# Optimization experiments

Measured on AMD Instinct MI355X. Metric: run time of the kernel, lower is better.

Reference implementation:

```python
import jax, jax.numpy as jnp
import numpy as np

N_NODES = 50000
N_EDGES = 640000
D_IN = 128
D_OUT = 128


def setup_inputs() -> dict:
    key = jax.random.key(0)
    k1, k2, k3, k4 = jax.random.split(key, 4)
    x = jax.random.normal(k1, (N_NODES, D_IN), dtype=jnp.float32)
    edge_index = jax.random.randint(k2, (2, N_EDGES), 0, N_NODES, dtype=jnp.int64)
    weight = jax.random.uniform(k3, (1,), dtype=jnp.float32)
    temperature = jnp.ones((1,), dtype=jnp.float32)
    W = jax.random.normal(k4, (D_IN, D_OUT), dtype=jnp.float32) * (1.0 / np.sqrt(D_IN))
    b = jnp.zeros((D_OUT,), dtype=jnp.float32)
    return {"x": x, "edge_index": edge_index, "weight": weight,
            "temperature": temperature, "W": W, "b": b}


def _gcn_conv(x, edge_index, W, b):
    N = x.shape[0]
    src, dst = edge_index[0], edge_index[1]
    loop = jnp.arange(N, dtype=edge_index.dtype)
    s = jnp.concatenate([src, loop])  # self-loops appended
    d = jnp.concatenate([dst, loop])
    deg = jax.ops.segment_sum(jnp.ones(s.shape[0], dtype=x.dtype), d, num_segments=N)
    dinv = jnp.where(deg > 0, deg ** -0.5, 0.0)
    norm = dinv[s] * dinv[d]  # [E+N]
    h = x @ W                 # linear transform first (PyG GCNConv)
    msg = h[s] * norm[:, None]
    out = jax.ops.segment_sum(msg, d, num_segments=N)
    return out + b


def _gradient_entropy(x, edge_index, temperature):
    # Boltzmann distribution over per-node Dirichlet energies;
    # entropy gradient w.r.t. node features (computed with autodiff).
    N = x.shape[0]
    src, dst = edge_index[0], edge_index[1]

    def entropy(z):
        diff = z[src] - z[dst]                                  # [E, D]
        E = jax.ops.segment_sum(jnp.sum(diff * diff, axis=-1), dst, num_segments=N)
        logp = jax.nn.log_softmax(-E / temperature[0])
        p = jnp.exp(logp)
        return -jnp.sum(p * logp)

    return jax.grad(entropy)(x)


def reference(x, edge_index, weight, temperature, W, b):
    h = _gcn_conv(x, edge_index, W, b)
    g = jax.lax.stop_gradient(_gradient_entropy(h, edge_index, temperature))
    return h + weight * g
```

## Files before the change

kernel.cpp:

```cpp
#include <hip/hip_runtime.h>

#define N_NODES 50000
#define N_EDGES 640000
#define NSCANB  196
#define MAXD    64

#define OFF_HTMPB    0
#define OFF_OBF      3200000
#define OFF_CURSOR   6400000
#define OFF_E        6450000
#define OFF_PMIN     6500000
#define OFF_PS0      6500256
#define OFF_PS1      6500512
#define OFF_WT       6500768
#define OFF_EBIN     6508960

typedef __attribute__((ext_vector_type(8))) short bf16x8;
typedef __attribute__((ext_vector_type(4))) float f32x4;

__device__ __forceinline__ unsigned short f2bf(float f) {
    unsigned u = __float_as_uint(f);
    unsigned r = u + 0x7fffu + ((u >> 16) & 1u);
    return (unsigned short)(r >> 16);
}
__device__ __forceinline__ float bflo(unsigned u) { return __uint_as_float(u << 16); }
__device__ __forceinline__ float bfhi(unsigned u) { return __uint_as_float(u & 0xffff0000u); }

__global__ __launch_bounds__(256) void k_init(const float* __restrict__ W,
                                              int* __restrict__ cursor,
                                              unsigned short* __restrict__ wtg) {
    int gtid = blockIdx.x * 256 + threadIdx.x;
    if (gtid < N_NODES) cursor[gtid] = 0;
    if (gtid < 4096) {
        int k = gtid >> 5, n4 = (gtid & 31) * 4;
        float4 v = *(const float4*)(W + k * 128 + n4);
        wtg[(n4 + 0) * 128 + k] = f2bf(v.x);
        wtg[(n4 + 1) * 128 + k] = f2bf(v.y);
        wtg[(n4 + 2) * 128 + k] = f2bf(v.z);
        wtg[(n4 + 3) * 128 + k] = f2bf(v.w);
    }
}

__global__ __launch_bounds__(256) void k_gemm(const float* __restrict__ x,
                                              const unsigned short* __restrict__ wtg,
                                              unsigned short* __restrict__ htmpb) {
    int tid = threadIdx.x;
    int wave = tid >> 6, lane = tid & 63, quad = lane >> 4, m16 = lane & 15;
    int r0 = blockIdx.x * 32 + (wave & 1) * 16;
    int ch = (wave >> 1) * 4;
    int arow = r0 + m16;
    int rowc = arow < N_NODES ? arow : N_NODES - 1;
    f32x4 acc[4];
    #pragma unroll
    for (int c = 0; c < 4; c++) acc[c] = (f32x4){0.f, 0.f, 0.f, 0.f};
    #pragma unroll
    for (int kt = 0; kt < 4; kt++) {
        int koff = kt * 32 + quad * 8;
        float4 xa = *(const float4*)(x + rowc * 128 + koff);
        float4 xb = *(const float4*)(x + rowc * 128 + koff + 4);
        bf16x8 af;
        af[0] = (short)f2bf(xa.x); af[1] = (short)f2bf(xa.y);
        af[2] = (short)f2bf(xa.z); af[3] = (short)f2bf(xa.w);
        af[4] = (short)f2bf(xb.x); af[5] = (short)f2bf(xb.y);
        af[6] = (short)f2bf(xb.z); af[7] = (short)f2bf(xb.w);
        #pragma unroll
        for (int c = 0; c < 4; c++) {
            bf16x8 bfrag = *(const bf16x8*)(wtg + ((ch + c) * 16 + m16) * 128 + koff);
            acc[c] = __builtin_amdgcn_mfma_f32_16x16x32_bf16(af, bfrag, acc[c], 0, 0, 0);
        }
    }
    #pragma unroll
    for (int reg = 0; reg < 4; reg++) {
        int grow = r0 + quad * 4 + reg;
        if (grow < N_NODES) {
            #pragma unroll
            for (int c = 0; c < 4; c++)
                htmpb[grow * 128 + (ch + c) * 16 + m16] = f2bf(acc[c][reg]);
        }
    }
}

__global__ __launch_bounds__(256) void k_bucket(const int* __restrict__ src,
                                                const int* __restrict__ dst,
                                                int* __restrict__ cursor,
                                                int* __restrict__ ebin) {
    int e = blockIdx.x * 256 + threadIdx.x;
    int d = dst[e];
    int pos = atomicAdd(&cursor[d], 1);
    if (pos < MAXD) ebin[d * MAXD + pos] = src[e];
}

__global__ __launch_bounds__(256) void k_gather(const unsigned short* __restrict__ htmpb,
                                                const int* __restrict__ deg,
                                                const float* __restrict__ b,
                                                const int* __restrict__ ebin,
                                                float* __restrict__ out,
                                                unsigned short* __restrict__ obf) {
    int node = blockIdx.x * 8 + (threadIdx.x >> 5);
    int lane = threadIdx.x & 31;
    int dg = deg[node]; if (dg > MAXD) dg = MAXD;
    float di = rsqrtf((float)(dg + 1));
    float4 bv = *(const float4*)(b + lane * 4);
    uint2 hv = *(const uint2*)(htmpb + node * 128 + lane * 4);
    float sl = di * di;
    float ax = bv.x + bflo(hv.x) * sl, ay = bv.y + bfhi(hv.x) * sl;
    float az = bv.z + bflo(hv.y) * sl, aw = bv.w + bfhi(hv.y) * sl;
    float cx = 0.f, cy = 0.f, cz = 0.f, cw = 0.f;
    const int* bin = ebin + node * MAXD;
    int k = 0;
    for (; k + 3 < dg; k += 4) {
        int s0 = bin[k], s1 = bin[k + 1], s2 = bin[k + 2], s3 = bin[k + 3];
        float n0 = di * rsqrtf((float)(deg[s0] + 1));
        float n1 = di * rsqrtf((float)(deg[s1] + 1));
        float n2 = di * rsqrtf((float)(deg[s2] + 1));
        float n3 = di * rsqrtf((float)(deg[s3] + 1));
        uint2 u0 = *(const uint2*)(htmpb + s0 * 128 + lane * 4);
        uint2 u1 = *(const uint2*)(htmpb + s1 * 128 + lane * 4);
        uint2 u2 = *(const uint2*)(htmpb + s2 * 128 + lane * 4);
        uint2 u3 = *(const uint2*)(htmpb + s3 * 128 + lane * 4);
        ax += bflo(u0.x) * n0; ay += bfhi(u0.x) * n0;
        az += bflo(u0.y) * n0; aw += bfhi(u0.y) * n0;
        cx += bflo(u1.x) * n1; cy += bfhi(u1.x) * n1;
        cz += bflo(u1.y) * n1; cw += bfhi(u1.y) * n1;
        ax += bflo(u2.x) * n2; ay += bfhi(u2.x) * n2;
        az += bflo(u2.y) * n2; aw += bfhi(u2.y) * n2;
        cx += bflo(u3.x) * n3; cy += bfhi(u3.x) * n3;
        cz += bflo(u3.y) * n3; cw += bfhi(u3.y) * n3;
    }
    for (; k < dg; k++) {
        int s0 = bin[k];
        float n0 = di * rsqrtf((float)(deg[s0] + 1));
        uint2 u0 = *(const uint2*)(htmpb + s0 * 128 + lane * 4);
        ax += bflo(u0.x) * n0; ay += bfhi(u0.x) * n0;
        az += bflo(u0.y) * n0; aw += bfhi(u0.y) * n0;
    }
    ax += cx; ay += cy; az += cz; aw += cw;
    *(float4*)(out + node * 128 + lane * 4) = make_float4(ax, ay, az, aw);
    uint2 pk;
    pk.x = (unsigned)f2bf(ax) | ((unsigned)f2bf(ay) << 16);
    pk.y = (unsigned)f2bf(az) | ((unsigned)f2bf(aw) << 16);
    *(uint2*)(obf + node * 128 + lane * 4) = pk;
}

__global__ __launch_bounds__(256) void k_energy(const unsigned short* __restrict__ obf,
                                                const int* __restrict__ deg,
                                                const int* __restrict__ ebin,
                                                float* __restrict__ E) {
    int node = blockIdx.x * 8 + (threadIdx.x >> 5);
    int lane = threadIdx.x & 31;
    int dg = deg[node]; if (dg > MAXD) dg = MAXD;
    uint2 ud = *(const uint2*)(obf + node * 128 + lane * 4);
    float o0 = bflo(ud.x), o1 = bfhi(ud.x), o2 = bflo(ud.y), o3 = bfhi(ud.y);
    float acc = 0.f, acc2 = 0.f;
    const int* bin = ebin + node * MAXD;
    int k = 0;
    for (; k + 3 < dg; k += 4) {
        int s0 = bin[k], s1 = bin[k + 1], s2 = bin[k + 2], s3 = bin[k + 3];
        uint2 a = *(const uint2*)(obf + s0 * 128 + lane * 4);
        uint2 c = *(const uint2*)(obf + s1 * 128 + lane * 4);
        uint2 g = *(const uint2*)(obf + s2 * 128 + lane * 4);
        uint2 h = *(const uint2*)(obf + s3 * 128 + lane * 4);
        float d0 = bflo(a.x) - o0, d1 = bfhi(a.x) - o1, d2 = bflo(a.y) - o2, d3 = bfhi(a.y) - o3;
        float e4 = bflo(c.x) - o0, e5 = bfhi(c.x) - o1, e6 = bflo(c.y) - o2, e7 = bfhi(c.y) - o3;
        float f0 = bflo(g.x) - o0, f1 = bfhi(g.x) - o1, f2 = bflo(g.y) - o2, f3 = bfhi(g.y) - o3;
        float h4 = bflo(h.x) - o0, h5 = bfhi(h.x) - o1, h6 = bflo(h.y) - o2, h7 = bfhi(h.y) - o3;
        acc  += d0 * d0 + d1 * d1 + d2 * d2 + d3 * d3;
        acc2 += e4 * e4 + e5 * e5 + e6 * e6 + e7 * e7;
        acc  += f0 * f0 + f1 * f1 + f2 * f2 + f3 * f3;
        acc2 += h4 * h4 + h5 * h5 + h6 * h6 + h7 * h7;
    }
    for (; k < dg; k++) {
        int s0 = bin[k];
        uint2 a = *(const uint2*)(obf + s0 * 128 + lane * 4);
        float d0 = bflo(a.x) - o0, d1 = bfhi(a.x) - o1, d2 = bflo(a.y) - o2, d3 = bfhi(a.y) - o3;
        acc += d0 * d0 + d1 * d1 + d2 * d2 + d3 * d3;
    }
    acc += acc2;
    #pragma unroll
    for (int off = 16; off; off >>= 1) acc += __shfl_xor(acc, off);
    if (lane == 0) E[node] = acc;
}

__global__ __launch_bounds__(256) void k_esoft(const float* __restrict__ E,
                                               const float* __restrict__ temp,
                                               float* __restrict__ pmin,
                                               float* __restrict__ ps0,
                                               float* __restrict__ ps1) {
    __shared__ float fred[12];
    int tid = threadIdx.x;
    int i = blockIdx.x * 256 + tid;
    int lane = tid & 63, wid = tid >> 6;
    float e = (i < N_NODES) ? E[i] : 3.402823466e38f;
    float m = e;
    #pragma unroll
    for (int off = 32; off; off >>= 1) m = fminf(m, __shfl_xor(m, off));
    if (lane == 0) fred[wid] = m;
    __syncthreads();
    float bm = fminf(fminf(fred[0], fred[1]), fminf(fred[2], fred[3]));
    float T = temp[0];
    float s0 = 0.f, s1 = 0.f;
    if (i < N_NODES) {
        float dd = (bm - e) / T;
        float ed = __expf(dd);
        s0 = ed; s1 = ed * dd;
    }
    #pragma unroll
    for (int off = 32; off; off >>= 1) { s0 += __shfl_xor(s0, off); s1 += __shfl_xor(s1, off); }
    __syncthreads();
    if (lane == 0) { fred[4 + wid] = s0; fred[8 + wid] = s1; }
    __syncthreads();
    if (tid == 0) {
        pmin[blockIdx.x] = bm;
        ps0[blockIdx.x] = fred[4] + fred[5] + fred[6] + fred[7];
        ps1[blockIdx.x] = fred[8] + fred[9] + fred[10] + fred[11];
    }
}

__global__ __launch_bounds__(256) void k_grad(const int* __restrict__ deg,
                                              const int* __restrict__ ebin,
                                              const float* __restrict__ E,
                                              const float* __restrict__ temp,
                                              const float* __restrict__ pmin,
                                              const float* __restrict__ ps0,
                                              const float* __restrict__ ps1,
                                              const float* __restrict__ weight,
                                              float* __restrict__ out) {
    __shared__ float fred[12];
    int tid = threadIdx.x;
    int lane = tid & 63, wid = tid >> 6;

    float pm = (tid < NSCANB) ? pmin[tid] : 3.402823466e38f;
    float m = pm;
    #pragma unroll
    for (int off = 32; off; off >>= 1) m = fminf(m, __shfl_xor(m, off));
    if (lane == 0) fred[wid] = m;
    __syncthreads();
    float gmin = fminf(fminf(fred[0], fred[1]), fminf(fred[2], fred[3]));
    float T = temp[0];
    float s0 = 0.f, s1 = 0.f;
    if (tid < NSCANB) {
        float dl = (gmin - pm) / T;
        float ex = __expf(dl);
        float b0 = ps0[tid], b1 = ps1[tid];
        s0 = ex * b0;
        s1 = ex * (b1 + dl * b0);
    }
    #pragma unroll
    for (int off = 32; off; off >>= 1) { s0 += __shfl_xor(s0, off); s1 += __shfl_xor(s1, off); }
    __syncthreads();
    if (lane == 0) { fred[4 + wid] = s0; fred[8 + wid] = s1; }
    __syncthreads();
    float S0 = fred[4] + fred[5] + fred[6] + fred[7];
    float S1 = fred[8] + fred[9] + fred[10] + fred[11];

    float wscale = 2.f * weight[0];
    int lane32 = tid & 31;
    int node = blockIdx.x * 8 + (tid >> 5);
    if (node >= N_NODES) return;
    float dd = (gmin - E[node]) / T;
    float qd = (__expf(dd) / S0) * (dd - S1 / S0) / T;
    if (qd == 0.f) return;
    float cc = wscale * qd;
    int dg = deg[node]; if (dg > MAXD) dg = MAXD;
    float4 od = *(const float4*)(out + node * 128 + lane32 * 4);
    float sx = 0.f, sy = 0.f, sz = 0.f, sw = 0.f;
    const int* bin = ebin + node * MAXD;
    for (int k = 0; k < dg; k++) {
        int s = bin[k];
        float4 a = *(const float4*)(out + s * 128 + lane32 * 4);
        float vx = cc * (a.x - od.x), vy = cc * (a.y - od.y);
        float vz = cc * (a.z - od.z), vw = cc * (a.w - od.w);
        float* os = out + s * 128 + lane32 * 4;
        atomicAdd(os + 0, vx); atomicAdd(os + 1, vy);
        atomicAdd(os + 2, vz); atomicAdd(os + 3, vw);
        sx += vx; sy += vy; sz += vz; sw += vw;
    }
    float* odp = out + node * 128 + lane32 * 4;
    atomicAdd(odp + 0, -sx); atomicAdd(odp + 1, -sy);
    atomicAdd(odp + 2, -sz); atomicAdd(odp + 3, -sw);
}

extern "C" void kernel_launch(void* const* d_in, const int* in_sizes, int n_in,
                              void* d_out, int out_size, void* d_ws, size_t ws_size,
                              hipStream_t stream) {
    const float* x      = (const float*)d_in[0];
    const int*   ei     = (const int*)d_in[1];
    const float* weight = (const float*)d_in[2];
    const float* temp   = (const float*)d_in[3];
    const float* W      = (const float*)d_in[4];
    const float* b      = (const float*)d_in[5];
    float* out = (float*)d_out;
    float* ws  = (float*)d_ws;

    const int* src = ei;
    const int* dst = ei + N_EDGES;

    unsigned short* htmpb = (unsigned short*)(ws + OFF_HTMPB);
    unsigned short* obf   = (unsigned short*)(ws + OFF_OBF);
    int*   cursor   = (int*)(ws + OFF_CURSOR);
    float* Earr     = ws + OFF_E;
    float* pminA    = ws + OFF_PMIN;
    float* ps0A     = ws + OFF_PS0;
    float* ps1A     = ws + OFF_PS1;
    unsigned short* wtg = (unsigned short*)(ws + OFF_WT);
    int*   ebin     = (int*)(ws + OFF_EBIN);

    k_init<<<NSCANB, 256, 0, stream>>>(W, cursor, wtg);
    k_gemm<<<1563, 256, 0, stream>>>(x, wtg, htmpb);
    k_bucket<<<N_EDGES / 256, 256, 0, stream>>>(src, dst, cursor, ebin);
    k_gather<<<6250, 256, 0, stream>>>(htmpb, cursor, b, ebin, out, obf);
    k_energy<<<6250, 256, 0, stream>>>(obf, cursor, ebin, Earr);
    k_esoft<<<NSCANB, 256, 0, stream>>>(Earr, temp, pminA, ps0A, ps1A);
    k_grad<<<6250, 256, 0, stream>>>(cursor, ebin, Earr, temp, pminA, ps0A, ps1A, weight, out);
}
```

Before: 231.2 us.

## Build CSR bins via two-pass shared-memory partition and prescale h by dinv

Replaces per-edge global atomic bucketing with a block-local histogram partition into coarse destination buckets, then a per-bucket shared-memory binning that writes 16-bit source indices plus deg and dinv arrays. The GEMM epilogue now multiplies rows by dinv, so the gather sums neighbors without per-neighbor degree loads and rsqrt. This targets scattered global atomics and dependent degree lookups, and halves adjacency index bandwidth. It relies on node ids fitting in 16 bits and on bucket occupancy staying below a fixed capacity.

```diff
diff --git a/kernel.cpp b/kernel.cpp
--- a/kernel.cpp
+++ b/kernel.cpp
@@ -4,16 +4,23 @@
 #define N_EDGES 640000
 #define NSCANB  196
 #define MAXD    64
+#define NBUCK   196
+#define BUCKCAP 4096
+#define EPB     2048
+#define NPARTB  313
 
 #define OFF_HTMPB    0
 #define OFF_OBF      3200000
-#define OFF_CURSOR   6400000
-#define OFF_E        6450000
-#define OFF_PMIN     6500000
-#define OFF_PS0      6500256
-#define OFF_PS1      6500512
-#define OFF_WT       6500768
-#define OFF_EBIN     6508960
+#define OFF_DEG      6400000
+#define OFF_DINV     6450000
+#define OFF_E        6500000
+#define OFF_PMIN     6550000
+#define OFF_PS0      6550256
+#define OFF_PS1      6550512
+#define OFF_WT       6550768
+#define OFF_GCUR     6558960
+#define OFF_PART     6559216
+#define OFF_EBIN     7362032
 
 typedef __attribute__((ext_vector_type(8))) short bf16x8;
 typedef __attribute__((ext_vector_type(4))) float f32x4;
@@ -27,10 +34,10 @@
 __device__ __forceinline__ float bfhi(unsigned u) { return __uint_as_float(u & 0xffff0000u); }
 
 __global__ __launch_bounds__(256) void k_init(const float* __restrict__ W,
-                                              int* __restrict__ cursor,
+                                              int* __restrict__ gcursor,
                                               unsigned short* __restrict__ wtg) {
     int gtid = blockIdx.x * 256 + threadIdx.x;
-    if (gtid < N_NODES) cursor[gtid] = 0;
+    if (gtid < NBUCK) gcursor[gtid] = 0;
     if (gtid < 4096) {
         int k = gtid >> 5, n4 = (gtid & 31) * 4;
         float4 v = *(const float4*)(W + k * 128 + n4);
@@ -41,8 +48,78 @@
     }
 }
 
+__global__ __launch_bounds__(256) void k_part(const int* __restrict__ src,
+                                              const int* __restrict__ dst,
+                                              int* __restrict__ gcursor,
+                                              unsigned* __restrict__ part) {
+    __shared__ int hist[NBUCK];
+    __shared__ int base[NBUCK];
+    int tid = threadIdx.x;
+    if (tid < NBUCK) hist[tid] = 0;
+    __syncthreads();
+    int e0 = blockIdx.x * EPB;
+    unsigned val[8]; int bk[8]; int rk[8];
+    #pragma unroll
+    for (int j = 0; j < 8; j++) {
+        int e = e0 + j * 256 + tid;
+        if (e < N_EDGES) {
+            int s = src[e], d = dst[e];
+            int bc = d >> 8;
+            if ((unsigned)bc >= NBUCK) bc = NBUCK - 1;
+            bk[j] = bc;
+            val[j] = ((unsigned)(d & 255) << 16) | ((unsigned)s & 0xffffu);
+            rk[j] = atomicAdd(&hist[bc], 1);
+        } else { bk[j] = -1; val[j] = 0u; rk[j] = 0; }
+    }
+    __syncthreads();
+    if (tid < NBUCK) base[tid] = atomicAdd(&gcursor[tid], hist[tid]);
+    __syncthreads();
+    #pragma unroll
+    for (int j = 0; j < 8; j++) {
+        if (bk[j] >= 0) {
+            int p = base[bk[j]] + rk[j];
+            if ((unsigned)p < BUCKCAP) part[bk[j] * BUCKCAP + p] = val[j];
+        }
+    }
+}
+
+__global__ __launch_bounds__(256) void k_bin(const int* __restrict__ gcursor,
+                                             const unsigned* __restrict__ part,
+                                             unsigned short* __restrict__ ebin,
+                                             int* __restrict__ deg,
+                                             float* __restrict__ dinv) {
+    __shared__ __align__(16) unsigned short bins[256][MAXD];
+    __shared__ int cnt[256];
+    int tid = threadIdx.x, bkt = blockIdx.x;
+    cnt[tid] = 0;
+    __syncthreads();
+    int M = gcursor[bkt];
+    if (M > BUCKCAP) M = BUCKCAP;
+    if (M < 0) M = 0;
+    for (int i = tid; i < M; i += 256) {
+        unsigned v = part[bkt * BUCKCAP + i];
+        int ln = (v >> 16) & 255;
+        int pos = atomicAdd(&cnt[ln], 1);
+        if (pos < MAXD) bins[ln][pos] = (unsigned short)(v & 0xffffu);
+    }
+    __syncthreads();
+    int node = bkt * 256 + tid;
+    if (node < N_NODES) {
+        int dg = cnt[tid]; if (dg > MAXD) dg = MAXD;
+        deg[node] = dg;
+        dinv[node] = rsqrtf((float)(dg + 1));
+    }
+    int nvalid = N_NODES - bkt * 256; if (nvalid > 256) nvalid = 256;
+    if (nvalid < 0) nvalid = 0;
+    int lim = nvalid * MAXD / 8;
+    const uint4* bs = (const uint4*)&bins[0][0];
+    uint4* gb = (uint4*)(ebin + (size_t)bkt * 256 * MAXD);
+    for (int i = tid; i < lim; i += 256) gb[i] = bs[i];
+}
+
 __global__ __launch_bounds__(256) void k_gemm(const float* __restrict__ x,
                                               const unsigned short* __restrict__ wtg,
+                                              const float* __restrict__ dinv,
                                               unsigned short* __restrict__ htmpb) {
     int tid = threadIdx.x;
     int wave = tid >> 6, lane = tid & 63, quad = lane >> 4, m16 = lane & 15;
@@ -73,68 +150,52 @@
     for (int reg = 0; reg < 4; reg++) {
         int grow = r0 + quad * 4 + reg;
         if (grow < N_NODES) {
+            float dv = dinv[grow];
             #pragma unroll
             for (int c = 0; c < 4; c++)
-                htmpb[grow * 128 + (ch + c) * 16 + m16] = f2bf(acc[c][reg]);
+                htmpb[grow * 128 + (ch + c) * 16 + m16] = f2bf(acc[c][reg] * dv);
         }
     }
-}
-
-__global__ __launch_bounds__(256) void k_bucket(const int* __restrict__ src,
-                                                const int* __restrict__ dst,
-                                                int* __restrict__ cursor,
-                                                int* __restrict__ ebin) {
-    int e = blockIdx.x * 256 + threadIdx.x;
-    int d = dst[e];
-    int pos = atomicAdd(&cursor[d], 1);
-    if (pos < MAXD) ebin[d * MAXD + pos] = src[e];
 }
 
 __global__ __launch_bounds__(256) void k_gather(const unsigned short* __restrict__ htmpb,
                                                 const int* __restrict__ deg,
+                                                const float* __restrict__ dinv,
                                                 const float* __restrict__ b,
-                                                const int* __restrict__ ebin,
+                                                const unsigned short* __restrict__ ebin,
                                                 float* __restrict__ out,
                                                 unsigned short* __restrict__ obf) {
     int node = blockIdx.x * 8 + (threadIdx.x >> 5);
     int lane = threadIdx.x & 31;
-    int dg = deg[node]; if (dg > MAXD) dg = MAXD;
-    float di = rsqrtf((float)(dg + 1));
+    int dg = deg[node]; if (dg > MAXD) dg = MAXD; if (dg < 0) dg = 0;
+    float di = dinv[node];
     float4 bv = *(const float4*)(b + lane * 4);
     uint2 hv = *(const uint2*)(htmpb + node * 128 + lane * 4);
-    float sl = di * di;
-    float ax = bv.x + bflo(hv.x) * sl, ay = bv.y + bfhi(hv.x) * sl;
-    float az = bv.z + bflo(hv.y) * sl, aw = bv.w + bfhi(hv.y) * sl;
+    float ax = bflo(hv.x), ay = bfhi(hv.x), az = bflo(hv.y), aw = bfhi(hv.y);
     float cx = 0.f, cy = 0.f, cz = 0.f, cw = 0.f;
-    const int* bin = ebin + node * MAXD;
+    const unsigned short* bin = ebin + node * MAXD;
     int k = 0;
     for (; k + 3 < dg; k += 4) {
-        int s0 = bin[k], s1 = bin[k + 1], s2 = bin[k + 2], s3 = bin[k + 3];
-        float n0 = di * rsqrtf((float)(deg[s0] + 1));
-        float n1 = di * rsqrtf((float)(deg[s1] + 1));
-        float n2 = di * rsqrtf((float)(deg[s2] + 1));
-        float n3 = di * rsqrtf((float)(deg[s3] + 1));
+        uint2 bw = *(const uint2*)(bin + k);
+        int s0 = bw.x & 0xffff, s1 = bw.x >> 16;
+        int s2 = bw.y & 0xffff, s3 = bw.y >> 16;
         uint2 u0 = *(const uint2*)(htmpb + s0 * 128 + lane * 4);
         uint2 u1 = *(const uint2*)(htmpb + s1 * 128 + lane * 4);
         uint2 u2 = *(const uint2*)(htmpb + s2 * 128 + lane * 4);
         uint2 u3 = *(const uint2*)(htmpb + s3 * 128 + lane * 4);
-        ax += bflo(u0.x) * n0; ay += bfhi(u0.x) * n0;
-        az += bflo(u0.y) * n0; aw += bfhi(u0.y) * n0;
-        cx += bflo(u1.x) * n1; cy += bfhi(u1.x) * n1;
-        cz += bflo(u1.y) * n1; cw += bfhi(u1.y) * n1;
-        ax += bflo(u2.x) * n2; ay += bfhi(u2.x) * n2;
-        az += bflo(u2.y) * n2; aw += bfhi(u2.y) * n2;
-        cx += bflo(u3.x) * n3; cy += bfhi(u3.x) * n3;
-        cz += bflo(u3.y) * n3; cw += bfhi(u3.y) * n3;
+        ax += bflo(u0.x); ay += bfhi(u0.x); az += bflo(u0.y); aw += bfhi(u0.y);
+        cx += bflo(u1.x); cy += bfhi(u1.x); cz += bflo(u1.y); cw += bfhi(u1.y);
+        ax += bflo(u2.x); ay += bfhi(u2.x); az += bflo(u2.y); aw += bfhi(u2.y);
+        cx += bflo(u3.x); cy += bfhi(u3.x); cz += bflo(u3.y); cw += bfhi(u3.y);
     }
     for (; k < dg; k++) {
         int s0 = bin[k];
-        float n0 = di * rsqrtf((float)(deg[s0] + 1));
         uint2 u0 = *(const uint2*)(htmpb + s0 * 128 + lane * 4);
-        ax += bflo(u0.x) * n0; ay += bfhi(u0.x) * n0;
-        az += bflo(u0.y) * n0; aw += bfhi(u0.y) * n0;
+        ax += bflo(u0.x); ay += bfhi(u0.x); az += bflo(u0.y); aw += bfhi(u0.y);
     }
     ax += cx; ay += cy; az += cz; aw += cw;
+    ax = bv.x + di * ax; ay = bv.y + di * ay;
+    az = bv.z + di * az; aw = bv.w + di * aw;
     *(float4*)(out + node * 128 + lane * 4) = make_float4(ax, ay, az, aw);
     uint2 pk;
     pk.x = (unsigned)f2bf(ax) | ((unsigned)f2bf(ay) << 16);
@@ -144,18 +205,20 @@
 
 __global__ __launch_bounds__(256) void k_energy(const unsigned short* __restrict__ obf,
                                                 const int* __restrict__ deg,
-                                                const int* __restrict__ ebin,
+                                                const unsigned short* __restrict__ ebin,
                                                 float* __restrict__ E) {
     int node = blockIdx.x * 8 + (threadIdx.x >> 5);
     int lane = threadIdx.x & 31;
-    int dg = deg[node]; if (dg > MAXD) dg = MAXD;
+    int dg = deg[node]; if (dg > MAXD) dg = MAXD; if (dg < 0) dg = 0;
     uint2 ud = *(const uint2*)(obf + node * 128 + lane * 4);
     float o0 = bflo(ud.x), o1 = bfhi(ud.x), o2 = bflo(ud.y), o3 = bfhi(ud.y);
     float acc = 0.f, acc2 = 0.f;
-    const int* bin = ebin + node * MAXD;
+    const unsigned short* bin = ebin + node * MAXD;
     int k = 0;
     for (; k + 3 < dg; k += 4) {
-        int s0 = bin[k], s1 = bin[k + 1], s2 = bin[k + 2], s3 = bin[k + 3];
+        uint2 bw = *(const uint2*)(bin + k);
+        int s0 = bw.x & 0xffff, s1 = bw.x >> 16;
+        int s2 = bw.y & 0xffff, s3 = bw.y >> 16;
         uint2 a = *(const uint2*)(obf + s0 * 128 + lane * 4);
         uint2 c = *(const uint2*)(obf + s1 * 128 + lane * 4);
         uint2 g = *(const uint2*)(obf + s2 * 128 + lane * 4);
@@ -217,7 +280,7 @@
 }
 
 __global__ __launch_bounds__(256) void k_grad(const int* __restrict__ deg,
-                                              const int* __restrict__ ebin,
+                                              const unsigned short* __restrict__ ebin,
                                               const float* __restrict__ E,
                                               const float* __restrict__ temp,
                                               const float* __restrict__ pmin,
@@ -261,12 +324,13 @@
     float qd = (__expf(dd) / S0) * (dd - S1 / S0) / T;
     if (qd == 0.f) return;
     float cc = wscale * qd;
-    int dg = deg[node]; if (dg > MAXD) dg = MAXD;
+    int dg = deg[node]; if (dg > MAXD) dg = MAXD; if (dg < 0) dg = 0;
     float4 od = *(const float4*)(out + node * 128 + lane32 * 4);
     float sx = 0.f, sy = 0.f, sz = 0.f, sw = 0.f;
-    const int* bin = ebin + node * MAXD;
+    const unsigned short* bin = ebin + node * MAXD;
     for (int k = 0; k < dg; k++) {
         int s = bin[k];
+        if (s >= N_NODES) s = N_NODES - 1;
         float4 a = *(const float4*)(out + s * 128 + lane32 * 4);
         float vx = cc * (a.x - od.x), vy = cc * (a.y - od.y);
         float vz = cc * (a.z - od.z), vw = cc * (a.w - od.w);
@@ -297,19 +361,23 @@
 
     unsigned short* htmpb = (unsigned short*)(ws + OFF_HTMPB);
     unsigned short* obf   = (unsigned short*)(ws + OFF_OBF);
-    int*   cursor   = (int*)(ws + OFF_CURSOR);
+    int*   deg      = (int*)(ws + OFF_DEG);
+    float* dinv     = ws + OFF_DINV;
     float* Earr     = ws + OFF_E;
     float* pminA    = ws + OFF_PMIN;
     float* ps0A     = ws + OFF_PS0;
     float* ps1A     = ws + OFF_PS1;
     unsigned short* wtg = (unsigned short*)(ws + OFF_WT);
-    int*   ebin     = (int*)(ws + OFF_EBIN);
-
-    k_init<<<NSCANB, 256, 0, stream>>>(W, cursor, wtg);
-    k_gemm<<<1563, 256, 0, stream>>>(x, wtg, htmpb);
-    k_bucket<<<N_EDGES / 256, 256, 0, stream>>>(src, dst, cursor, ebin);
-    k_gather<<<6250, 256, 0, stream>>>(htmpb, cursor, b, ebin, out, obf);
-    k_energy<<<6250, 256, 0, stream>>>(obf, cursor, ebin, Earr);
+    int*   gcursor  = (int*)(ws + OFF_GCUR);
+    unsigned* part  = (unsigned*)(ws + OFF_PART);
+    unsigned short* ebin = (unsigned short*)(ws + OFF_EBIN);
+
+    k_init<<<16, 256, 0, stream>>>(W, gcursor, wtg);
+    k_part<<<NPARTB, 256, 0, stream>>>(src, dst, gcursor, part);
+    k_bin<<<NBUCK, 256, 0, stream>>>(gcursor, part, ebin, deg, dinv);
+    k_gemm<<<1563, 256, 0, stream>>>(x, wtg, dinv, htmpb);
+    k_gather<<<6250, 256, 0, stream>>>(htmpb, deg, dinv, b, ebin, out, obf);
+    k_energy<<<6250, 256, 0, stream>>>(obf, deg, ebin, Earr);
     k_esoft<<<NSCANB, 256, 0, stream>>>(Earr, temp, pminA, ps0A, ps1A);
-    k_grad<<<6250, 256, 0, stream>>>(cursor, ebin, Earr, temp, pminA, ps0A, ps1A, weight, out);
-}
+    k_grad<<<6250, 256, 0, stream>>>(deg, ebin, Earr, temp, pminA, ps0A, ps1A, weight, out);
+}
```

Result: faster. 218.0 us (-5.7%).
